# Kernel optimization log

Hardware: AMD Instinct MI355X
Metric: run time of the kernel (lower is better)

## Reference

```python
import jax, jax.numpy as jnp
import numpy as np

N_NODES = 50000
N_EDGES = 500000
F_DIM = 128
N_REL = 8
N_LAYERS = 2
NEG_SLOPE = 0.2  # PyG RGATConv default negative_slope


def setup_inputs() -> dict:
    key = jax.random.key(0)
    ks = jax.random.split(key, 6)
    x = jax.random.normal(ks[0], (N_NODES, F_DIM), dtype=jnp.float32)
    edge_index = jax.random.randint(ks[1], (2, N_EDGES), 0, N_NODES)
    edge_type = jax.random.randint(ks[2], (N_EDGES,), 0, N_REL)
    # Per-layer relation weights [L, R, F_in, F_out], attention vectors q,k [L, F_out, 1], bias [L, F_out]
    W = jax.random.normal(ks[3], (N_LAYERS, N_REL, F_DIM, F_DIM), dtype=jnp.float32) * (1.0 / np.sqrt(F_DIM)).astype(np.float32)
    att_q = jax.random.normal(ks[4], (N_LAYERS, F_DIM, 1), dtype=jnp.float32) * 0.1
    att_k = jax.random.normal(ks[5], (N_LAYERS, F_DIM, 1), dtype=jnp.float32) * 0.1
    bias = jnp.zeros((N_LAYERS, F_DIM), dtype=jnp.float32)
    return {"x": x, "W": W, "att_q": att_q, "att_k": att_k, "bias": bias,
            "edge_index": edge_index, "edge_type": edge_type}


def _segment_softmax(logits, seg, num_segments):
    # Numerically stable softmax over edges grouped by destination node.
    m = jax.ops.segment_max(logits, seg, num_segments=num_segments)
    m = jax.lax.stop_gradient(m)
    e = jnp.exp(logits - m[seg])
    denom = jax.ops.segment_sum(e, seg, num_segments=num_segments)
    return e / (denom[seg] + 1e-16)


def _rgat_layer(h, src, dst, edge_type, W, q, k, b):
    # h: [N, F]; W: [R, F, F]. Project once per relation, then gather per edge
    # (avoids materializing [E, F, F] per-edge weight gathers).
    n = h.shape[0]
    xw = jnp.einsum('nf,rfg->rng', h, W)          # [R, N, F]
    out_j = xw[edge_type, src]                    # [E, F] transformed source feats
    out_i = xw[edge_type, dst]                    # [E, F] transformed dest feats
    # additive self-attention: leaky_relu(q(x_i) + k(x_j)), heads=1, dim=1
    logits = jax.nn.leaky_relu((out_i @ q + out_j @ k)[:, 0], NEG_SLOPE)  # [E]
    alpha = _segment_softmax(logits, dst, n)      # across-relation softmax per dst node
    agg = jax.ops.segment_sum(alpha[:, None] * out_j, dst, num_segments=n)  # [N, F]
    return agg + b


def reference(x, W, att_q, att_k, bias, edge_index, edge_type):
    src, dst = edge_index[0], edge_index[1]
    h = x
    for l in range(W.shape[0]):  # small fixed layer count
        h = _rgat_layer(h, src, dst, edge_type, W[l], att_q[l], att_k[l], bias[l])
        h = jax.nn.relu(h)  # dropout is identity in eval mode
    return h
```

## Files before the change

kernel.cpp:

```cpp
#include <hip/hip_runtime.h>
#include <hip/hip_bf16.h>
#include <hip/hip_fp16.h>

#define N_NODES 50000
#define N_EDGES 500000
#define F_DIM   128
#define N_REL   8
#define N_LAYERS 2
#define NEG_SLOPE 0.2f

#define NBLK_N ((N_NODES + 255) / 256)

typedef _Float16 half8 __attribute__((ext_vector_type(8)));
typedef float f32x4  __attribute__((ext_vector_type(4)));


__device__ inline float lrelu(float l) { return (l > 0.f) ? l : NEG_SLOPE * l; }

__global__ __launch_bounds__(256) void prep_h(const float* __restrict__ H,
                                              _Float16* __restrict__ Hf) {
    const size_t i8 = (size_t)blockIdx.x * 256 + threadIdx.x;
    if (i8 >= (size_t)N_NODES * F_DIM / 8) return;
    const float* src = H + i8 * 8;
    float av[8];
    *(float4*)(av)     = *(const float4*)(src);
    *(float4*)(av + 4) = *(const float4*)(src + 4);
    alignas(16) _Float16 hb[8];
#pragma unroll
    for (int j = 0; j < 8; ++j) hb[j] = (_Float16)av[j];
    *(uint4*)(Hf + i8 * 8) = *(const uint4*)hb;
}

__global__ __launch_bounds__(256) void prep_w(const float* __restrict__ W,
                                              _Float16* __restrict__ Wf) {
    __shared__ float tile[64][F_DIM + 1];
    const int mat = blockIdx.x;
    const float* src = W + (size_t)mat * F_DIM * F_DIM;
    const int t = threadIdx.x;
    for (int hf = 0; hf < 2; ++hf) {
#pragma unroll
        for (int i = 0; i < 8; ++i) {
            int idx = t + i * 256;
            int f = idx >> 5, c4 = idx & 31;
            float4 v = *(const float4*)(src + (size_t)(hf * 64 + f) * F_DIM + c4 * 4);
            *(float4*)&tile[f][c4 * 4] = v;
        }
        __syncthreads();
        int g = t >> 1, fs = (t & 1) * 32;
        for (int c = 0; c < 4; ++c) {
            alignas(16) _Float16 th[8];
#pragma unroll
            for (int j = 0; j < 8; ++j) th[j] = (_Float16)tile[fs + c * 8 + j][g];
            size_t o = ((size_t)mat * F_DIM + g) * F_DIM + hf * 64 + fs + c * 8;
            *(uint4*)(Wf + o) = *(const uint4*)th;
        }
        __syncthreads();
    }
}

#define GBM 256
__global__ __launch_bounds__(256, 2) void gemm_xw(const _Float16* __restrict__ Hf,
                                                  const _Float16* __restrict__ Wf,
                                                  const float* __restrict__ qv_g,
                                                  const float* __restrict__ kv_g,
                                                  __half* __restrict__ xw,
                                                  float* __restrict__ a_q,
                                                  float* __restrict__ a_k) {
    __shared__ _Float16 lds[F_DIM * F_DIM];
    const int r   = blockIdx.y;
    const int tid = threadIdx.x;
    const int lane = tid & 63, w = tid >> 6;
    const int q = lane >> 4, ln = lane & 15;

    {
        const _Float16* src = Wf + (size_t)r * F_DIM * F_DIM;
#pragma unroll
        for (int i = 0; i < 8; ++i) {
            int chunk = tid + i * 256;
            int gg = chunk >> 4, c8 = chunk & 15;
            uint4 v = *(const uint4*)(src + gg * F_DIM + c8 * 8);
            *(uint4*)(lds + gg * F_DIM + ((c8 ^ (gg & 15)) * 8)) = v;
        }
    }

    float qvl[8], kvl[8];
#pragma unroll
    for (int t = 0; t < 8; ++t) {
        qvl[t] = qv_g[t * 16 + ln];
        kvl[t] = kv_g[t * 16 + ln];
    }

    __syncthreads();

    for (int t4 = 0; t4 < 2; ++t4) {
        const int rb0 = blockIdx.x * GBM + t4 * 128;
        if (rb0 >= N_NODES) break;

        half8 Af[2][4];
#pragma unroll
        for (int rt = 0; rt < 2; ++rt) {
            int row = rb0 + w * 32 + rt * 16 + ln;
            int ar = (row < N_NODES) ? row : (N_NODES - 1);
            const _Float16* hp = Hf + (size_t)ar * F_DIM;
#pragma unroll
            for (int ks = 0; ks < 4; ++ks)
                Af[rt][ks] = *(const half8*)(hp + ks * 32 + q * 8);
        }

        f32x4 acc[2][8];
#pragma unroll
        for (int rt = 0; rt < 2; ++rt)
#pragma unroll
            for (int t = 0; t < 8; ++t) acc[rt][t] = (f32x4)(0.f);

#pragma unroll
        for (int ks = 0; ks < 4; ++ks) {
            const int jx = (((ks * 4 + q) ^ ln)) << 3;
            half8 Bf[8];
#pragma unroll
            for (int c = 0; c < 8; ++c)
                Bf[c] = *(const half8*)(lds + (c * 16 + ln) * F_DIM + jx);
#pragma unroll
            for (int c = 0; c < 8; ++c)
#pragma unroll
                for (int rt = 0; rt < 2; ++rt)
                    acc[rt][c] = __builtin_amdgcn_mfma_f32_16x16x32_f16(Af[rt][ks], Bf[c], acc[rt][c], 0, 0, 0);
        }

#pragma unroll
        for (int rt = 0; rt < 2; ++rt) {
            float pq[4], pk[4];
#pragma unroll
            for (int reg = 0; reg < 4; ++reg) {
                const int row = rb0 + w * 32 + rt * 16 + q * 4 + reg;
                alignas(16) unsigned short hs[8];
                float sq = 0.f, sk = 0.f;
#pragma unroll
                for (int t = 0; t < 8; ++t) {
                    float v = acc[rt][t][reg];
                    __half hv = __float2half(v);
                    hs[t] = *reinterpret_cast<unsigned short*>(&hv);
                    sq = fmaf(v, qvl[t], sq);
                    sk = fmaf(v, kvl[t], sk);
                }
                if (row < N_NODES)
                    *(uint4*)(xw + ((size_t)r * N_NODES + row) * F_DIM + ln * 8) = *(const uint4*)hs;
                pq[reg] = sq; pk[reg] = sk;
            }
#pragma unroll
            for (int reg = 0; reg < 4; ++reg) {
#pragma unroll
                for (int m = 1; m <= 8; m <<= 1) {
                    pq[reg] += __shfl_xor(pq[reg], m);
                    pk[reg] += __shfl_xor(pk[reg], m);
                }
            }
            if (ln == 0) {
#pragma unroll
                for (int reg = 0; reg < 4; ++reg) {
                    const int row = rb0 + w * 32 + rt * 16 + q * 4 + reg;
                    if (row < N_NODES) {
                        a_q[r * N_NODES + row] = pq[reg];
                        a_k[r * N_NODES + row] = pk[reg];
                    }
                }
            }
        }
    }
}


__global__ __launch_bounds__(256) void count_kernel(const int* __restrict__ dstp,
                                                    int* __restrict__ cnt) {
    int e = blockIdx.x * 256 + threadIdx.x;
    if (e < N_EDGES) atomicAdd(cnt + dstp[e], 1);
}

__global__ __launch_bounds__(256) void block_sum_kernel(const int* __restrict__ cnt,
                                                        int* __restrict__ partial) {
    __shared__ int s[256];
    int idx = blockIdx.x * 256 + threadIdx.x;
    int v = (idx < N_NODES) ? cnt[idx] : 0;
    s[threadIdx.x] = v;
    __syncthreads();
    for (int off = 128; off > 0; off >>= 1) {
        if (threadIdx.x < off) s[threadIdx.x] += s[threadIdx.x + off];
        __syncthreads();
    }
    if (threadIdx.x == 0) partial[blockIdx.x] = s[0];
}

__global__ __launch_bounds__(256) void scan_partials_kernel(int* __restrict__ partial,
                                                            int* __restrict__ row_ptr) {
    __shared__ int s[256];
    int t = threadIdx.x;
    int v = (t < NBLK_N) ? partial[t] : 0;
    s[t] = v;
    __syncthreads();
#pragma unroll
    for (int off = 1; off < 256; off <<= 1) {
        int x = (t >= off) ? s[t - off] : 0;
        __syncthreads();
        s[t] += x;
        __syncthreads();
    }
    if (t < NBLK_N) partial[t] = s[t] - v;
    if (t == 0) row_ptr[N_NODES] = N_EDGES;
}

__global__ __launch_bounds__(256) void scan_block_kernel(const int* __restrict__ cnt,
                                                         const int* __restrict__ partial,
                                                         int* __restrict__ row_ptr) {
    __shared__ int s[256];
    int t = threadIdx.x;
    int idx = blockIdx.x * 256 + t;
    int v = (idx < N_NODES) ? cnt[idx] : 0;
    s[t] = v;
    __syncthreads();
#pragma unroll
    for (int off = 1; off < 256; off <<= 1) {
        int x = (t >= off) ? s[t - off] : 0;
        __syncthreads();
        s[t] += x;
        __syncthreads();
    }
    if (idx < N_NODES) row_ptr[idx] = partial[blockIdx.x] + s[t] - v;
}

__global__ __launch_bounds__(256) void scatter_kernel(const int* __restrict__ srcp,
                                                      const int* __restrict__ dstp,
                                                      const int* __restrict__ etp,
                                                      const int* __restrict__ row_ptr,
                                                      int* __restrict__ cursor,
                                                      unsigned* __restrict__ sorted,
                                                      unsigned short* __restrict__ dst16) {
    int e = blockIdx.x * 256 + threadIdx.x;
    if (e >= N_EDGES) return;
    int d = dstp[e];
    int pos = atomicAdd(cursor + d, 1);
    int j = row_ptr[d] + pos;
    sorted[j] = (unsigned)srcp[e] | ((unsigned)etp[e] << 16);
    dst16[j] = (unsigned short)d;
}

__global__ __launch_bounds__(256) void logits_kernel(const float* __restrict__ a_q,
                                                     const float* __restrict__ a_k,
                                                     const unsigned* __restrict__ sorted,
                                                     const unsigned short* __restrict__ dst16,
                                                     float* __restrict__ lgt) {
    int j = blockIdx.x * 256 + threadIdx.x;
    if (j >= N_EDGES) return;
    unsigned p = sorted[j];
    int s = p & 0xffff, t = p >> 16;
    int d = dst16[j];
    lgt[j] = lrelu(a_q[t * N_NODES + d] + a_k[t * N_NODES + s]);
}

__device__ inline void accum8(float* acc, uint4 v, float a) {
    const __half2* h2 = reinterpret_cast<const __half2*>(&v);
#pragma unroll
    for (int t = 0; t < 4; ++t) {
        float2 f = __half22float2(h2[t]);
        acc[t * 2]     = fmaf(a, f.x, acc[t * 2]);
        acc[t * 2 + 1] = fmaf(a, f.y, acc[t * 2 + 1]);
    }
}
__device__ inline const uint4* xwrow(const __half* xw, unsigned p, int ln) {
    return (const uint4*)(xw + (((size_t)(p >> 16)) * N_NODES + (p & 0xffff)) * F_DIM + ln * 8);
}

__global__ __launch_bounds__(256) void agg_fused(const __half* __restrict__ xw,
                                                 const float* __restrict__ lgt,
                                                 const int* __restrict__ row_ptr,
                                                 const unsigned* __restrict__ sorted,
                                                 const float* __restrict__ bias,
                                                 float* __restrict__ outp,
                                                 _Float16* __restrict__ hfp) {
    const int lane = threadIdx.x & 63;
    const int wave = threadIdx.x >> 6;
    const int half = lane >> 5, hl = lane & 31;
    const int d0 = blockIdx.x * 8 + wave * 2;
    if (d0 >= N_NODES) return;
    const int dmy = d0 + half;
    const int dv = (dmy < N_NODES) ? dmy : (N_NODES - 1);
    const int beg = row_ptr[dv], end = row_ptr[dv + 1];
    int cnt = (dmy < N_NODES) ? (end - beg) : 0;
    const int cntO = __shfl_xor(cnt, 32);
    const int cmax = (cnt > cntO) ? cnt : cntO;

    if (cmax <= 32) {
        unsigned p = 0;
        float ex = 0.f;
        if (hl < cnt) {
            p = sorted[beg + hl];
            ex = __expf(lgt[beg + hl]);
        }

        const int gg = hl >> 4, ln = hl & 15;
        float acc[8] = {0, 0, 0, 0, 0, 0, 0, 0};
        for (int i = 0; i < cnt; i += 8) {
            unsigned p0 = __shfl(p, i + gg, 32);
            unsigned p1 = __shfl(p, i + 2 + gg, 32);
            unsigned p2 = __shfl(p, i + 4 + gg, 32);
            unsigned p3 = __shfl(p, i + 6 + gg, 32);
            float a0 = __shfl(ex, i + gg, 32);
            float a1 = __shfl(ex, i + 2 + gg, 32);
            float a2 = __shfl(ex, i + 4 + gg, 32);
            float a3 = __shfl(ex, i + 6 + gg, 32);
            uint4 v0 = *xwrow(xw, p0, ln);
            uint4 v1 = *xwrow(xw, p1, ln);
            uint4 v2 = *xwrow(xw, p2, ln);
            uint4 v3 = *xwrow(xw, p3, ln);
            accum8(acc, v0, a0);
            accum8(acc, v1, a1);
            accum8(acc, v2, a2);
            accum8(acc, v3, a3);
        }
        float dsum = ex;
#pragma unroll
        for (int off = 16; off > 0; off >>= 1) dsum += __shfl_xor(dsum, off, 32);
#pragma unroll
        for (int t = 0; t < 8; ++t) acc[t] += __shfl_xor(acc[t], 16, 32);

        if (dmy < N_NODES) {
            const float inv = 1.f / (dsum + 1e-16f);
#pragma unroll
            for (int j = 0; j < 4; ++j) {
                const int t = gg * 4 + j;
                const int col = t * 16 + ln;
                const float v = fmaxf(fmaf(acc[t], inv, bias[col]), 0.f);
                if (outp) outp[(size_t)dmy * F_DIM + col] = v;
                if (hfp)  hfp[(size_t)dmy * F_DIM + col] = (_Float16)v;
            }
        }
    } else {
        const int g = lane >> 4, ln = lane & 15;
        for (int h = 0; h < 2; ++h) {
            const int dd = d0 + h;
            if (dd >= N_NODES) continue;
            const int b = __shfl(beg, h * 32);
            const int c = __shfl(cnt, h * 32);
            if (c <= 64) {
                unsigned p = 0;
                float l = -3.4e38f;
                if (lane < c) {
                    p = sorted[b + lane];
                    l = lgt[b + lane];
                }
                float m = l;
#pragma unroll
                for (int off = 32; off > 0; off >>= 1) m = fmaxf(m, __shfl_xor(m, off));
                const float ex = (lane < c) ? __expf(l - m) : 0.f;
                float acc[8] = {0, 0, 0, 0, 0, 0, 0, 0};
                for (int i = 0; i < c; i += 8) {
                    unsigned p0 = __shfl(p, i + g);
                    unsigned p1 = __shfl(p, i + 4 + g);
                    float a0 = __shfl(ex, i + g);
                    float a1 = __shfl(ex, i + 4 + g);
                    uint4 v0 = *xwrow(xw, p0, ln);
                    uint4 v1 = *xwrow(xw, p1, ln);
                    accum8(acc, v0, a0);
                    accum8(acc, v1, a1);
                }
                float dsum = ex;
#pragma unroll
                for (int off = 32; off > 0; off >>= 1) dsum += __shfl_xor(dsum, off);
#pragma unroll
                for (int t = 0; t < 8; ++t) {
                    acc[t] += __shfl_xor(acc[t], 16);
                    acc[t] += __shfl_xor(acc[t], 32);
                }
                const float inv = 1.f / (dsum + 1e-16f);
#pragma unroll
                for (int j = 0; j < 2; ++j) {
                    const int t = g * 2 + j;
                    const int col = t * 16 + ln;
                    const float v = fmaxf(fmaf(acc[t], inv, bias[col]), 0.f);
                    if (outp) outp[(size_t)dd * F_DIM + col] = v;
                    if (hfp)  hfp[(size_t)dd * F_DIM + col] = (_Float16)v;
                }
            } else {
                const int p0 = lane * 2;
                const int c0 = (p0 & 7) * 16 + (p0 >> 3);
                const int c1 = c0 + 16;
                float2 acc = make_float2(bias[c0], bias[c1]);
                float m = -3.4e38f;
                for (int i = b + lane; i < b + c; i += 64) m = fmaxf(m, lgt[i]);
#pragma unroll
                for (int off = 32; off > 0; off >>= 1) m = fmaxf(m, __shfl_xor(m, off));
                float dsum = 0.f;
                for (int i = b + lane; i < b + c; i += 64) dsum += __expf(lgt[i] - m);
#pragma unroll
                for (int off = 32; off > 0; off >>= 1) dsum += __shfl_xor(dsum, off);
                const float inv = 1.f / (dsum + 1e-16f);
                for (int i = b; i < b + c; ++i) {
                    unsigned pp = sorted[i];
                    float alpha = __expf(lgt[i] - m) * inv;
                    const __half2 h2 = *((const __half2*)xw + (((size_t)(pp >> 16)) * N_NODES + (pp & 0xffff)) * (F_DIM / 2) + lane);
                    float2 v = make_float2(__half2float(h2.x), __half2float(h2.y));
                    acc.x = fmaf(alpha, v.x, acc.x);
                    acc.y = fmaf(alpha, v.y, acc.y);
                }
                const float v0 = fmaxf(acc.x, 0.f), v1 = fmaxf(acc.y, 0.f);
                if (outp) { outp[(size_t)dd * F_DIM + c0] = v0; outp[(size_t)dd * F_DIM + c1] = v1; }
                if (hfp)  { hfp[(size_t)dd * F_DIM + c0] = (_Float16)v0; hfp[(size_t)dd * F_DIM + c1] = (_Float16)v1; }
            }
        }
    }
}


extern "C" void kernel_launch(void* const* d_in, const int* in_sizes, int n_in,
                              void* d_out, int out_size, void* d_ws, size_t ws_size,
                              hipStream_t stream) {
    const float* x     = (const float*)d_in[0];
    const float* W     = (const float*)d_in[1];
    const float* att_q = (const float*)d_in[2];
    const float* att_k = (const float*)d_in[3];
    const float* bias  = (const float*)d_in[4];
    const int* ei      = (const int*)d_in[5];
    const int* etp     = (const int*)d_in[6];
    const int* srcp = ei;
    const int* dstp = ei + N_EDGES;
    float* out = (float*)d_out;
    char* ws   = (char*)d_ws;

    size_t off = 0;
    auto alloc = [&](size_t bytes) {
        void* p = ws + off;
        off = (off + bytes + 511) & ~(size_t)511;
        return p;
    };
    __half* xw       = (__half*)alloc((size_t)N_REL * N_NODES * F_DIM * sizeof(__half));
    float* a_q       = (float*)alloc((size_t)N_REL * N_NODES * sizeof(float));
    float* a_k       = (float*)alloc((size_t)N_REL * N_NODES * sizeof(float));
    int* cnt         = (int*)alloc((size_t)2 * N_NODES * sizeof(int));
    int* cursor      = cnt + N_NODES;
    int* row_ptr     = (int*)alloc(((size_t)N_NODES + 1) * sizeof(int));
    int* partial     = (int*)alloc(256 * sizeof(int));
    unsigned* sorted = (unsigned*)alloc((size_t)N_EDGES * sizeof(unsigned));
    unsigned short* dst16 = (unsigned short*)alloc((size_t)N_EDGES * sizeof(unsigned short));
    float* lgt       = (float*)alloc((size_t)N_EDGES * sizeof(float));
    _Float16* Wf     = (_Float16*)alloc((size_t)N_LAYERS * N_REL * F_DIM * F_DIM * sizeof(_Float16));
    _Float16* Hf     = (_Float16*)alloc((size_t)N_NODES * F_DIM * sizeof(_Float16));

    prep_w<<<N_LAYERS * N_REL, 256, 0, stream>>>(W, Wf);
    hipMemsetAsync(cnt, 0, (size_t)2 * N_NODES * 4, stream);
    count_kernel<<<(N_EDGES + 255) / 256, 256, 0, stream>>>(dstp, cnt);
    block_sum_kernel<<<NBLK_N, 256, 0, stream>>>(cnt, partial);
    scan_partials_kernel<<<1, 256, 0, stream>>>(partial, row_ptr);
    scan_block_kernel<<<NBLK_N, 256, 0, stream>>>(cnt, partial, row_ptr);
    scatter_kernel<<<(N_EDGES + 255) / 256, 256, 0, stream>>>(
        srcp, dstp, etp, row_ptr, cursor, sorted, dst16);

    const int grid_h = (N_NODES * F_DIM / 8 + 255) / 256;
    const int grid_m = (N_NODES + GBM - 1) / GBM;
    const int grid_e = (N_EDGES + 255) / 256;
    prep_h<<<grid_h, 256, 0, stream>>>(x, Hf);
    for (int l = 0; l < N_LAYERS; ++l) {
        gemm_xw<<<dim3(grid_m, N_REL), 256, 0, stream>>>(
            Hf, Wf + (size_t)l * N_REL * F_DIM * F_DIM,
            att_q + l * F_DIM, att_k + l * F_DIM,
            xw, a_q, a_k);
        logits_kernel<<<grid_e, 256, 0, stream>>>(a_q, a_k, sorted, dst16, lgt);
        const bool last = (l == N_LAYERS - 1);
        agg_fused<<<(N_NODES + 7) / 8, 256, 0, stream>>>(
            xw, lgt, row_ptr, sorted, bias + l * F_DIM,
            last ? out : nullptr,
            last ? nullptr : Hf);
    }
}
```

Measured before the change: 279.4 us.

## Fuse logits into aggregation and fp32 input conversion into first GEMM

Removes the separate logits kernel and computes each edge's exponentiated attention score directly inside the aggregation kernel from the per-node a_q/a_k arrays. Also drops the segment-max subtraction, relying on logits staying small enough to avoid overflow. Removes the prep_h conversion kernel by having the first-layer GEMM read fp32 inputs and convert to fp16 in registers. This saves kernel launches and the intermediate logit and dst16 buffers, but recomputes gathers and exps for high-degree nodes and loses overflow protection for large logits.

```diff
diff --git a/kernel.cpp b/kernel.cpp
--- a/kernel.cpp
+++ b/kernel.cpp
@@ -16,20 +16,6 @@
 
 
 __device__ inline float lrelu(float l) { return (l > 0.f) ? l : NEG_SLOPE * l; }
-
-__global__ __launch_bounds__(256) void prep_h(const float* __restrict__ H,
-                                              _Float16* __restrict__ Hf) {
-    const size_t i8 = (size_t)blockIdx.x * 256 + threadIdx.x;
-    if (i8 >= (size_t)N_NODES * F_DIM / 8) return;
-    const float* src = H + i8 * 8;
-    float av[8];
-    *(float4*)(av)     = *(const float4*)(src);
-    *(float4*)(av + 4) = *(const float4*)(src + 4);
-    alignas(16) _Float16 hb[8];
-#pragma unroll
-    for (int j = 0; j < 8; ++j) hb[j] = (_Float16)av[j];
-    *(uint4*)(Hf + i8 * 8) = *(const uint4*)hb;
-}
 
 __global__ __launch_bounds__(256) void prep_w(const float* __restrict__ W,
                                               _Float16* __restrict__ Wf) {
@@ -60,6 +46,8 @@
 
 #define GBM 256
 __global__ __launch_bounds__(256, 2) void gemm_xw(const _Float16* __restrict__ Hf,
+                                                  const float* __restrict__ Hx,
+                                                  const int use32,
                                                   const _Float16* __restrict__ Wf,
                                                   const float* __restrict__ qv_g,
                                                   const float* __restrict__ kv_g,
@@ -101,10 +89,23 @@
         for (int rt = 0; rt < 2; ++rt) {
             int row = rb0 + w * 32 + rt * 16 + ln;
             int ar = (row < N_NODES) ? row : (N_NODES - 1);
-            const _Float16* hp = Hf + (size_t)ar * F_DIM;
-#pragma unroll
-            for (int ks = 0; ks < 4; ++ks)
-                Af[rt][ks] = *(const half8*)(hp + ks * 32 + q * 8);
+            if (use32) {
+                const float* hp = Hx + (size_t)ar * F_DIM;
+#pragma unroll
+                for (int ks = 0; ks < 4; ++ks) {
+                    float4 f0 = *(const float4*)(hp + ks * 32 + q * 8);
+                    float4 f1 = *(const float4*)(hp + ks * 32 + q * 8 + 4);
+                    alignas(16) _Float16 hb[8] = {
+                        (_Float16)f0.x, (_Float16)f0.y, (_Float16)f0.z, (_Float16)f0.w,
+                        (_Float16)f1.x, (_Float16)f1.y, (_Float16)f1.z, (_Float16)f1.w};
+                    Af[rt][ks] = *(const half8*)hb;
+                }
+            } else {
+                const _Float16* hp = Hf + (size_t)ar * F_DIM;
+#pragma unroll
+                for (int ks = 0; ks < 4; ++ks)
+                    Af[rt][ks] = *(const half8*)(hp + ks * 32 + q * 8);
+            }
         }
 
         f32x4 acc[2][8];
@@ -232,28 +233,12 @@
                                                       const int* __restrict__ etp,
                                                       const int* __restrict__ row_ptr,
                                                       int* __restrict__ cursor,
-                                                      unsigned* __restrict__ sorted,
-                                                      unsigned short* __restrict__ dst16) {
+                                                      unsigned* __restrict__ sorted) {
     int e = blockIdx.x * 256 + threadIdx.x;
     if (e >= N_EDGES) return;
     int d = dstp[e];
     int pos = atomicAdd(cursor + d, 1);
-    int j = row_ptr[d] + pos;
-    sorted[j] = (unsigned)srcp[e] | ((unsigned)etp[e] << 16);
-    dst16[j] = (unsigned short)d;
-}
-
-__global__ __launch_bounds__(256) void logits_kernel(const float* __restrict__ a_q,
-                                                     const float* __restrict__ a_k,
-                                                     const unsigned* __restrict__ sorted,
-                                                     const unsigned short* __restrict__ dst16,
-                                                     float* __restrict__ lgt) {
-    int j = blockIdx.x * 256 + threadIdx.x;
-    if (j >= N_EDGES) return;
-    unsigned p = sorted[j];
-    int s = p & 0xffff, t = p >> 16;
-    int d = dst16[j];
-    lgt[j] = lrelu(a_q[t * N_NODES + d] + a_k[t * N_NODES + s]);
+    sorted[row_ptr[d] + pos] = (unsigned)srcp[e] | ((unsigned)etp[e] << 16);
 }
 
 __device__ inline void accum8(float* acc, uint4 v, float a) {
@@ -268,9 +253,15 @@
 __device__ inline const uint4* xwrow(const __half* xw, unsigned p, int ln) {
     return (const uint4*)(xw + (((size_t)(p >> 16)) * N_NODES + (p & 0xffff)) * F_DIM + ln * 8);
 }
+__device__ inline float edge_ex(const float* a_q, const float* a_k,
+                                unsigned p, int d) {
+    int s = p & 0xffff, t = p >> 16;
+    return __expf(lrelu(a_q[t * N_NODES + d] + a_k[t * N_NODES + s]));
+}
 
 __global__ __launch_bounds__(256) void agg_fused(const __half* __restrict__ xw,
-                                                 const float* __restrict__ lgt,
+                                                 const float* __restrict__ a_q,
+                                                 const float* __restrict__ a_k,
                                                  const int* __restrict__ row_ptr,
                                                  const unsigned* __restrict__ sorted,
                                                  const float* __restrict__ bias,
@@ -293,7 +284,7 @@
         float ex = 0.f;
         if (hl < cnt) {
             p = sorted[beg + hl];
-            ex = __expf(lgt[beg + hl]);
+            ex = edge_ex(a_q, a_k, p, dmy);
         }
 
         const int gg = hl >> 4, ln = hl & 15;
@@ -342,15 +333,11 @@
             const int c = __shfl(cnt, h * 32);
             if (c <= 64) {
                 unsigned p = 0;
-                float l = -3.4e38f;
+                float ex = 0.f;
                 if (lane < c) {
                     p = sorted[b + lane];
-                    l = lgt[b + lane];
-                }
-                float m = l;
-#pragma unroll
-                for (int off = 32; off > 0; off >>= 1) m = fmaxf(m, __shfl_xor(m, off));
-                const float ex = (lane < c) ? __expf(l - m) : 0.f;
+                    ex = edge_ex(a_q, a_k, p, dd);
+                }
                 float acc[8] = {0, 0, 0, 0, 0, 0, 0, 0};
                 for (int i = 0; i < c; i += 8) {
                     unsigned p0 = __shfl(p, i + g);
@@ -384,23 +371,23 @@
                 const int c0 = (p0 & 7) * 16 + (p0 >> 3);
                 const int c1 = c0 + 16;
                 float2 acc = make_float2(bias[c0], bias[c1]);
-                float m = -3.4e38f;
-                for (int i = b + lane; i < b + c; i += 64) m = fmaxf(m, lgt[i]);
-#pragma unroll
-                for (int off = 32; off > 0; off >>= 1) m = fmaxf(m, __shfl_xor(m, off));
                 float dsum = 0.f;
-                for (int i = b + lane; i < b + c; i += 64) dsum += __expf(lgt[i] - m);
+                for (int i = b + lane; i < b + c; i += 64)
+                    dsum += edge_ex(a_q, a_k, sorted[i], dd);
 #pragma unroll
                 for (int off = 32; off > 0; off >>= 1) dsum += __shfl_xor(dsum, off);
                 const float inv = 1.f / (dsum + 1e-16f);
+                float sx = 0.f, sy = 0.f;
                 for (int i = b; i < b + c; ++i) {
                     unsigned pp = sorted[i];
-                    float alpha = __expf(lgt[i] - m) * inv;
+                    float alpha = edge_ex(a_q, a_k, pp, dd);
                     const __half2 h2 = *((const __half2*)xw + (((size_t)(pp >> 16)) * N_NODES + (pp & 0xffff)) * (F_DIM / 2) + lane);
                     float2 v = make_float2(__half2float(h2.x), __half2float(h2.y));
-                    acc.x = fmaf(alpha, v.x, acc.x);
-                    acc.y = fmaf(alpha, v.y, acc.y);
-                }
+                    sx = fmaf(alpha, v.x, sx);
+                    sy = fmaf(alpha, v.y, sy);
+                }
+                acc.x += sx * inv;
+                acc.y += sy * inv;
                 const float v0 = fmaxf(acc.x, 0.f), v1 = fmaxf(acc.y, 0.f);
                 if (outp) { outp[(size_t)dd * F_DIM + c0] = v0; outp[(size_t)dd * F_DIM + c1] = v1; }
                 if (hfp)  { hfp[(size_t)dd * F_DIM + c0] = (_Float16)v0; hfp[(size_t)dd * F_DIM + c1] = (_Float16)v1; }
@@ -439,8 +426,6 @@
     int* row_ptr     = (int*)alloc(((size_t)N_NODES + 1) * sizeof(int));
     int* partial     = (int*)alloc(256 * sizeof(int));
     unsigned* sorted = (unsigned*)alloc((size_t)N_EDGES * sizeof(unsigned));
-    unsigned short* dst16 = (unsigned short*)alloc((size_t)N_EDGES * sizeof(unsigned short));
-    float* lgt       = (float*)alloc((size_t)N_EDGES * sizeof(float));
     _Float16* Wf     = (_Float16*)alloc((size_t)N_LAYERS * N_REL * F_DIM * F_DIM * sizeof(_Float16));
     _Float16* Hf     = (_Float16*)alloc((size_t)N_NODES * F_DIM * sizeof(_Float16));
 
@@ -451,21 +436,18 @@
     scan_partials_kernel<<<1, 256, 0, stream>>>(partial, row_ptr);
     scan_block_kernel<<<NBLK_N, 256, 0, stream>>>(cnt, partial, row_ptr);
     scatter_kernel<<<(N_EDGES + 255) / 256, 256, 0, stream>>>(
-        srcp, dstp, etp, row_ptr, cursor, sorted, dst16);
-
-    const int grid_h = (N_NODES * F_DIM / 8 + 255) / 256;
+        srcp, dstp, etp, row_ptr, cursor, sorted);
+
     const int grid_m = (N_NODES + GBM - 1) / GBM;
-    const int grid_e = (N_EDGES + 255) / 256;
-    prep_h<<<grid_h, 256, 0, stream>>>(x, Hf);
     for (int l = 0; l < N_LAYERS; ++l) {
         gemm_xw<<<dim3(grid_m, N_REL), 256, 0, stream>>>(
-            Hf, Wf + (size_t)l * N_REL * F_DIM * F_DIM,
+            Hf, x, (l == 0) ? 1 : 0,
+            Wf + (size_t)l * N_REL * F_DIM * F_DIM,
             att_q + l * F_DIM, att_k + l * F_DIM,
             xw, a_q, a_k);
-        logits_kernel<<<grid_e, 256, 0, stream>>>(a_q, a_k, sorted, dst16, lgt);
         const bool last = (l == N_LAYERS - 1);
         agg_fused<<<(N_NODES + 7) / 8, 256, 0, stream>>>(
-            xw, lgt, row_ptr, sorted, bias + l * F_DIM,
+            xw, a_q, a_k, row_ptr, sorted, bias + l * F_DIM,
             last ? out : nullptr,
             last ? nullptr : Hf);
     }
```

Result: no change. 279.9 us (+0.2%).
